# Performance work log

Measured on AMD Instinct MI355X. Metric: run time of the kernel, lower is better.

## Reference

```python
import jax, jax.numpy as jnp
import numpy as np

E = 32      # particle_embed_dim = q/k/v head out dim
G = 2       # nof_net_types (conv groups)
NEG_SLOPE = 0.01


def _glin(x, w, b, groups):
    """Grouped 1x1 conv on (M, C, 1, 1) == grouped linear.
    x: (M, Cin), w: (Cout, Cin//groups), b: (Cout,)."""
    M = x.shape[0]
    Cout = w.shape[0]
    xg = x.reshape(M, groups, -1)                 # (M, G, Cin/G)
    wg = w.reshape(groups, Cout // groups, -1)    # (G, Cout/G, Cin/G)
    y = jnp.einsum('mgi,goi->mgo', xg, wg).reshape(M, Cout)
    return y + b


def setup_inputs() -> dict:
    key = jax.random.key(0)
    ks = jax.random.split(key, 9)
    B, N = 32, 1024
    s = 0.05
    return {
        'x_e':   jax.random.normal(ks[0], (B, N, G * E), dtype=jnp.float32),
        'w_qkv': jax.random.normal(ks[1], (3 * G * E, E), dtype=jnp.float32) * s,
        'b_qkv': jax.random.normal(ks[2], (3 * G * E,), dtype=jnp.float32) * s,
        'w_h1':  jax.random.normal(ks[3], (G * E, 2 * E), dtype=jnp.float32) * s,
        'b_h1':  jax.random.normal(ks[4], (G * E,), dtype=jnp.float32) * s,
        'w_h10': jax.random.normal(ks[5], (G * E, E), dtype=jnp.float32) * s,
        'b_h10': jax.random.normal(ks[6], (G * E,), dtype=jnp.float32) * s,
        'w_h11': jax.random.normal(ks[7], (G * E, E), dtype=jnp.float32) * s,
        'b_h11': jax.random.normal(ks[8], (G * E,), dtype=jnp.float32) * s,
    }


def reference(x_e, w_qkv, b_qkv, w_h1, b_h1, w_h10, b_h10, w_h11, b_h11):
    B, N, D = x_e.shape                      # D = G*E = 64
    act = lambda z: jnp.where(z >= 0, z, NEG_SLOPE * z)

    # grouped 1x1-conv QKV projection
    qkv = _glin(x_e.reshape(B * N, D), w_qkv, b_qkv, G)        # (B*N, 3*G*E)
    qkv = qkv.reshape(B, N, G, 3, E).transpose(0, 2, 3, 1, 4)  # (B, G, 3, N, E)
    q, k, v = qkv[:, :, 0], qkv[:, :, 1], qkv[:, :, 2]         # each (B, G, N, E)

    # NOTE: module divides k by sqrt(E) and logits by sqrt(E) again -> 1/E total
    scale = 1.0 / E
    ip = jnp.einsum('bgne,bgme->bgnm', q, k) * scale           # (B, G, N, N)
    sip = jax.nn.softmax(ip, axis=-1)
    attn = jnp.einsum('bgnm,bgme->bgne', sip, v)               # (B, G, N, E)

    # concat pre-attention v with attention output, regroup per-particle
    x_xe = jnp.concatenate([v, attn], axis=3)                  # (B, G, N, 2E)
    x_xe = x_xe.transpose(0, 2, 1, 3).reshape(B * N, G * 2 * E)  # (B*N, 128)

    h = act(_glin(x_xe, w_h1, b_h1, G))
    h = act(_glin(h, w_h10, b_h10, G))
    h = act(_glin(h, w_h11, b_h11, G))
    return h.reshape(B * N, G * E, 1, 1)
```

## Files before the change

kernel.cpp:

```cpp
#include <hip/hip_runtime.h>

#define B_ 32
#define N_ 1024
#define NEG 0.01f
#define QSC (1.4426950408889634f/32.0f)

using half8  = __attribute__((ext_vector_type(8))) _Float16;
using half4  = __attribute__((ext_vector_type(4))) _Float16;
using floatx4 = __attribute__((ext_vector_type(4))) float;

#if defined(__has_builtin)
#if __has_builtin(__builtin_amdgcn_exp2f)
#define EXP2(x) __builtin_amdgcn_exp2f(x)
#endif
#endif
#ifndef EXP2
#define EXP2(x) exp2f(x)
#endif

__device__ inline half8 cvt8(float4 a, float4 b) {
    half8 h;
    h[0]=(_Float16)a.x; h[1]=(_Float16)a.y; h[2]=(_Float16)a.z; h[3]=(_Float16)a.w;
    h[4]=(_Float16)b.x; h[5]=(_Float16)b.y; h[6]=(_Float16)b.z; h[7]=(_Float16)b.w;
    return h;
}

struct __align__(16) Smem {
    _Float16 wsh[96*36];
    float    bsh[96];
    _Float16 Kst[128*40];
    _Float16 Vtst[32*136];
    union {
        _Float16 qs[128*40];
        _Float16 xs[128*72];
    } u;
    float linv[128];
    float bl1[32], bl10[32], bl11[32];
};

__global__ __launch_bounds__(256, 2) void fused_kernel(
    const float* __restrict__ x, const float* __restrict__ w_qkv, const float* __restrict__ b_qkv,
    const float* __restrict__ w_h1,  const float* __restrict__ b_h1,
    const float* __restrict__ w_h10, const float* __restrict__ b_h10,
    const float* __restrict__ w_h11, const float* __restrict__ b_h11,
    float* __restrict__ out)
{
    __shared__ Smem sm;
    int t = threadIdx.x;
    int bg = blockIdx.x >> 3;
    int qtile = blockIdx.x & 7;
    int b = bg >> 1, g = bg & 1;
    int qbase = qtile * 128;
    int lane = t & 63, w = t >> 6;
    int L15 = lane & 15, quad = lane >> 4;

    for (int idx = t; idx < 96*32; idx += 256) {
        int r = idx >> 5, c = idx & 31;
        sm.wsh[r*36 + c] = (_Float16)w_qkv[(g*96 + r)*32 + c];
    }
    if (t < 96) sm.bsh[t] = b_qkv[g*96 + t];
    if (t < 32) {
        sm.bl1[t]  = b_h1[g*32+t];
        sm.bl10[t] = b_h10[g*32+t];
        sm.bl11[t] = b_h11[g*32+t];
    }
    __syncthreads();

    half8 bwq[2], bwk[2], bwv[2];
    float bqv[2], bkv[2], bvv[2];
    #pragma unroll
    for (int et = 0; et < 2; et++) {
        bwq[et] = *(const half8*)&sm.wsh[(     et*16 + L15)*36 + quad*8];
        bwk[et] = *(const half8*)&sm.wsh[(32 + et*16 + L15)*36 + quad*8];
        bwv[et] = *(const half8*)&sm.wsh[(64 + et*16 + L15)*36 + quad*8];
        bqv[et] = sm.bsh[     et*16 + L15];
        bkv[et] = sm.bsh[32 + et*16 + L15];
        bvv[et] = sm.bsh[64 + et*16 + L15];
    }

    {
        floatx4 z = {0.f,0.f,0.f,0.f};
        floatx4 dq[2][2];
        #pragma unroll
        for (int mt = 0; mt < 2; mt++) {
            const float* p = x + ((size_t)b*N_ + qbase + w*32 + mt*16 + L15)*64 + g*32 + quad*8;
            float4 f0 = *(const float4*)p;
            float4 f1 = *(const float4*)(p + 4);
            half8 axq = cvt8(f0, f1);
            dq[mt][0] = __builtin_amdgcn_mfma_f32_16x16x32_f16(axq, bwq[0], z, 0,0,0);
            dq[mt][1] = __builtin_amdgcn_mfma_f32_16x16x32_f16(axq, bwq[1], z, 0,0,0);
        }
        #pragma unroll
        for (int mt = 0; mt < 2; mt++)
            #pragma unroll
            for (int et = 0; et < 2; et++)
                #pragma unroll
                for (int r = 0; r < 4; r++)
                    sm.u.qs[(w*32 + mt*16 + quad*4 + r)*40 + et*16 + L15] =
                        (_Float16)((dq[mt][et][r] + bqv[et])*QSC);
    }
    __syncthreads();
    half8 bq0 = *(const half8*)&sm.u.qs[(w*32 +      L15)*40 + quad*8];
    half8 bq1 = *(const half8*)&sm.u.qs[(w*32 + 16 + L15)*40 + quad*8];

    float4 xf0[2], xf1[2];
    #pragma unroll
    for (int mt = 0; mt < 2; mt++) {
        const float* p = x + ((size_t)b*N_ + 0*128 + w*32 + mt*16 + L15)*64 + g*32 + quad*8;
        xf0[mt] = *(const float4*)p;
        xf1[mt] = *(const float4*)(p + 4);
    }

    floatx4 o00 = {0.f,0.f,0.f,0.f}, o01 = o00, o10 = o00, o11 = o00;
    float lsum0 = 0.f, lsum1 = 0.f;

    for (int kt = 0; kt < 8; kt++) {
        floatx4 z = {0.f,0.f,0.f,0.f};
        floatx4 dK[2][2], dV[2][2];
        #pragma unroll
        for (int mt = 0; mt < 2; mt++) {
            half8 axk = cvt8(xf0[mt], xf1[mt]);
            dK[mt][0] = __builtin_amdgcn_mfma_f32_16x16x32_f16(axk, bwk[0], z, 0,0,0);
            dK[mt][1] = __builtin_amdgcn_mfma_f32_16x16x32_f16(axk, bwk[1], z, 0,0,0);
            dV[mt][0] = __builtin_amdgcn_mfma_f32_16x16x32_f16(axk, bwv[0], z, 0,0,0);
            dV[mt][1] = __builtin_amdgcn_mfma_f32_16x16x32_f16(axk, bwv[1], z, 0,0,0);
        }
        __syncthreads();
        #pragma unroll
        for (int mt = 0; mt < 2; mt++) {
            int rb = w*32 + mt*16 + quad*4;
            #pragma unroll
            for (int et = 0; et < 2; et++) {
                half4 vh;
                #pragma unroll
                for (int r = 0; r < 4; r++) {
                    sm.Kst[(rb + r)*40 + et*16 + L15] = (_Float16)(dK[mt][et][r] + bkv[et]);
                    vh[r] = (_Float16)(dV[mt][et][r] + bvv[et]);
                }
                *(half4*)&sm.Vtst[(et*16 + L15)*136 + rb] = vh;
                if (kt == qtile) {
                    #pragma unroll
                    for (int r = 0; r < 4; r++)
                        sm.u.xs[(rb + r)*72 + et*16 + L15] = vh[r];
                }
            }
        }
        __syncthreads();
        if (kt < 7) {
            #pragma unroll
            for (int mt = 0; mt < 2; mt++) {
                const float* p = x + ((size_t)b*N_ + (kt+1)*128 + w*32 + mt*16 + L15)*64 + g*32 + quad*8;
                xf0[mt] = *(const float4*)p;
                xf1[mt] = *(const float4*)(p + 4);
            }
        }
        #pragma unroll
        for (int mt8 = 0; mt8 < 8; mt8++) {
            half8 ak = *(const half8*)&sm.Kst[(mt8*16 + L15)*40 + quad*8];
            floatx4 zz = {0.f,0.f,0.f,0.f};
            floatx4 s0 = __builtin_amdgcn_mfma_f32_16x16x32_f16(ak, bq0, zz, 0,0,0);
            floatx4 s1 = __builtin_amdgcn_mfma_f32_16x16x32_f16(ak, bq1, zz, 0,0,0);
            float p00 = EXP2(s0.x), p01 = EXP2(s0.y), p02 = EXP2(s0.z), p03 = EXP2(s0.w);
            float p10 = EXP2(s1.x), p11 = EXP2(s1.y), p12 = EXP2(s1.z), p13 = EXP2(s1.w);
            lsum0 += (p00+p01)+(p02+p03);
            lsum1 += (p10+p11)+(p12+p13);
            half4 a0 = { (_Float16)p00, (_Float16)p01, (_Float16)p02, (_Float16)p03 };
            half4 a1 = { (_Float16)p10, (_Float16)p11, (_Float16)p12, (_Float16)p13 };
            half4 bv0 = *(const half4*)&sm.Vtst[      L15*136 + mt8*16 + quad*4];
            half4 bv1 = *(const half4*)&sm.Vtst[(16 + L15)*136 + mt8*16 + quad*4];
            o00 = __builtin_amdgcn_mfma_f32_16x16x16f16(a0, bv0, o00, 0,0,0);
            o01 = __builtin_amdgcn_mfma_f32_16x16x16f16(a0, bv1, o01, 0,0,0);
            o10 = __builtin_amdgcn_mfma_f32_16x16x16f16(a1, bv0, o10, 0,0,0);
            o11 = __builtin_amdgcn_mfma_f32_16x16x16f16(a1, bv1, o11, 0,0,0);
        }
    }

    lsum0 += __shfl_xor(lsum0, 16, 64); lsum0 += __shfl_xor(lsum0, 32, 64);
    lsum1 += __shfl_xor(lsum1, 16, 64); lsum1 += __shfl_xor(lsum1, 32, 64);
    if (quad == 0) {
        sm.linv[w*32 +      L15] = 1.0f / lsum0;
        sm.linv[w*32 + 16 + L15] = 1.0f / lsum1;
    }
    __syncthreads();

    {
        const floatx4* ofr[2][2] = { {&o00,&o01}, {&o10,&o11} };
        #pragma unroll
        for (int nt = 0; nt < 2; nt++) {
            float4 li = *(const float4*)&sm.linv[w*32 + nt*16 + quad*4];
            #pragma unroll
            for (int et = 0; et < 2; et++) {
                floatx4 ov = *ofr[nt][et];
                sm.u.xs[(w*32+nt*16+quad*4+0)*72 + 32 + et*16 + L15] = (_Float16)(ov[0]*li.x);
                sm.u.xs[(w*32+nt*16+quad*4+1)*72 + 32 + et*16 + L15] = (_Float16)(ov[1]*li.y);
                sm.u.xs[(w*32+nt*16+quad*4+2)*72 + 32 + et*16 + L15] = (_Float16)(ov[2]*li.z);
                sm.u.xs[(w*32+nt*16+quad*4+3)*72 + 32 + et*16 + L15] = (_Float16)(ov[3]*li.w);
            }
        }
    }
    __syncthreads();

    half4 a1f[2][4], a2f[2][2], a3f[2][2];
    #pragma unroll
    for (int mt = 0; mt < 2; mt++) {
        #pragma unroll
        for (int kt = 0; kt < 4; kt++) {
            float4 f = *(const float4*)(w_h1 + (size_t)(g*32+mt*16+L15)*64 + kt*16 + quad*4);
            half4 h = { (_Float16)f.x, (_Float16)f.y, (_Float16)f.z, (_Float16)f.w };
            a1f[mt][kt] = h;
        }
        #pragma unroll
        for (int kt = 0; kt < 2; kt++) {
            float4 f = *(const float4*)(w_h10 + (size_t)(g*32+mt*16+L15)*32 + kt*16 + quad*4);
            half4 h = { (_Float16)f.x, (_Float16)f.y, (_Float16)f.z, (_Float16)f.w };
            a2f[mt][kt] = h;
            float4 f2 = *(const float4*)(w_h11 + (size_t)(g*32+mt*16+L15)*32 + kt*16 + quad*4);
            half4 h2 = { (_Float16)f2.x, (_Float16)f2.y, (_Float16)f2.z, (_Float16)f2.w };
            a3f[mt][kt] = h2;
        }
    }

    floatx4 d1[2][2];
    #pragma unroll
    for (int mt = 0; mt < 2; mt++)
        #pragma unroll
        for (int nt = 0; nt < 2; nt++) d1[mt][nt] = (floatx4){0.f,0.f,0.f,0.f};
    #pragma unroll
    for (int nt = 0; nt < 2; nt++)
        #pragma unroll
        for (int kt = 0; kt < 4; kt++) {
            half4 b1 = *(const half4*)&sm.u.xs[(w*32+nt*16+L15)*72 + kt*16 + quad*4];
            d1[0][nt] = __builtin_amdgcn_mfma_f32_16x16x16f16(a1f[0][kt], b1, d1[0][nt], 0,0,0);
            d1[1][nt] = __builtin_amdgcn_mfma_f32_16x16x16f16(a1f[1][kt], b1, d1[1][nt], 0,0,0);
        }
    half4 h1b[2][2];
    #pragma unroll
    for (int mt = 0; mt < 2; mt++) {
        float4 bb = *(const float4*)&sm.bl1[mt*16 + quad*4];
        #pragma unroll
        for (int nt = 0; nt < 2; nt++) {
            float v0 = d1[mt][nt][0] + bb.x; v0 = (v0>=0.f)?v0:NEG*v0;
            float v1 = d1[mt][nt][1] + bb.y; v1 = (v1>=0.f)?v1:NEG*v1;
            float v2 = d1[mt][nt][2] + bb.z; v2 = (v2>=0.f)?v2:NEG*v2;
            float v3 = d1[mt][nt][3] + bb.w; v3 = (v3>=0.f)?v3:NEG*v3;
            half4 h = { (_Float16)v0, (_Float16)v1, (_Float16)v2, (_Float16)v3 };
            h1b[mt][nt] = h;
        }
    }
    floatx4 d2[2][2];
    #pragma unroll
    for (int mt = 0; mt < 2; mt++)
        #pragma unroll
        for (int nt = 0; nt < 2; nt++) d2[mt][nt] = (floatx4){0.f,0.f,0.f,0.f};
    #pragma unroll
    for (int mt = 0; mt < 2; mt++)
        #pragma unroll
        for (int nt = 0; nt < 2; nt++)
            #pragma unroll
            for (int kt = 0; kt < 2; kt++)
                d2[mt][nt] = __builtin_amdgcn_mfma_f32_16x16x16f16(a2f[mt][kt], h1b[kt][nt], d2[mt][nt], 0,0,0);
    half4 h2b[2][2];
    #pragma unroll
    for (int mt = 0; mt < 2; mt++) {
        float4 bb = *(const float4*)&sm.bl10[mt*16 + quad*4];
        #pragma unroll
        for (int nt = 0; nt < 2; nt++) {
            float v0 = d2[mt][nt][0] + bb.x; v0 = (v0>=0.f)?v0:NEG*v0;
            float v1 = d2[mt][nt][1] + bb.y; v1 = (v1>=0.f)?v1:NEG*v1;
            float v2 = d2[mt][nt][2] + bb.z; v2 = (v2>=0.f)?v2:NEG*v2;
            float v3 = d2[mt][nt][3] + bb.w; v3 = (v3>=0.f)?v3:NEG*v3;
            half4 h = { (_Float16)v0, (_Float16)v1, (_Float16)v2, (_Float16)v3 };
            h2b[mt][nt] = h;
        }
    }
    floatx4 d3[2][2];
    #pragma unroll
    for (int mt = 0; mt < 2; mt++)
        #pragma unroll
        for (int nt = 0; nt < 2; nt++) d3[mt][nt] = (floatx4){0.f,0.f,0.f,0.f};
    #pragma unroll
    for (int mt = 0; mt < 2; mt++)
        #pragma unroll
        for (int nt = 0; nt < 2; nt++)
            #pragma unroll
            for (int kt = 0; kt < 2; kt++)
                d3[mt][nt] = __builtin_amdgcn_mfma_f32_16x16x16f16(a3f[mt][kt], h2b[kt][nt], d3[mt][nt], 0,0,0);
    #pragma unroll
    for (int mt = 0; mt < 2; mt++) {
        float4 bb = *(const float4*)&sm.bl11[mt*16 + quad*4];
        #pragma unroll
        for (int nt = 0; nt < 2; nt++) {
            float4 ov;
            ov.x = d3[mt][nt][0] + bb.x; ov.x = (ov.x>=0.f)?ov.x:NEG*ov.x;
            ov.y = d3[mt][nt][1] + bb.y; ov.y = (ov.y>=0.f)?ov.y:NEG*ov.y;
            ov.z = d3[mt][nt][2] + bb.z; ov.z = (ov.z>=0.f)?ov.z:NEG*ov.z;
            ov.w = d3[mt][nt][3] + bb.w; ov.w = (ov.w>=0.f)?ov.w:NEG*ov.w;
            *(float4*)(out + ((size_t)b*N_ + qbase + w*32 + nt*16 + L15)*64 + g*32 + mt*16 + quad*4) = ov;
        }
    }
}

extern "C" void kernel_launch(void* const* d_in, const int* in_sizes, int n_in,
                              void* d_out, int out_size, void* d_ws, size_t ws_size,
                              hipStream_t stream) {
    const float* x_e   = (const float*)d_in[0];
    const float* w_qkv = (const float*)d_in[1];
    const float* b_qkv = (const float*)d_in[2];
    const float* w_h1  = (const float*)d_in[3];
    const float* b_h1  = (const float*)d_in[4];
    const float* w_h10 = (const float*)d_in[5];
    const float* b_h10 = (const float*)d_in[6];
    const float* w_h11 = (const float*)d_in[7];
    const float* b_h11 = (const float*)d_in[8];
    float* out = (float*)d_out;

    hipLaunchKernelGGL(fused_kernel, dim3(B_*2*8), dim3(256), 0, stream,
                       x_e, w_qkv, b_qkv, w_h1, b_h1, w_h10, b_h10, w_h11, b_h11, out);
}
```

Baseline: 100.1 us.

## Double-buffer K/V tiles in LDS, fold biases into MFMA accumulators, use packed fp16 converts

K/V shared-memory tiles are double-buffered so the projection of the next key tile runs after the current tile's attention MFMAs, leaving one barrier per iteration instead of two. Biases are now seeded into the MFMA accumulators, and the Q scale is folded into the Q weights and bias, which removes per-element adds and multiplies. Scalar float-to-half conversions are replaced with packed round-toward-zero conversions (cvt_pkrtz). The cost is extra LDS for the second buffers, which may affect the 2-blocks-per-CU occupancy, plus a small rounding-mode difference.

```diff
diff --git a/kernel.cpp b/kernel.cpp
--- a/kernel.cpp
+++ b/kernel.cpp
@@ -7,6 +7,8 @@
 
 using half8  = __attribute__((ext_vector_type(8))) _Float16;
 using half4  = __attribute__((ext_vector_type(4))) _Float16;
+using half2  = __attribute__((ext_vector_type(2))) _Float16;
+using fp16x2 = __attribute__((ext_vector_type(2))) __fp16;
 using floatx4 = __attribute__((ext_vector_type(4))) float;
 
 #if defined(__has_builtin)
@@ -18,18 +20,25 @@
 #define EXP2(x) exp2f(x)
 #endif
 
+__device__ inline half2 pkcvt(float a, float b) {
+    fp16x2 r = __builtin_amdgcn_cvt_pkrtz(a, b);
+    return __builtin_bit_cast(half2, r);
+}
+
 __device__ inline half8 cvt8(float4 a, float4 b) {
-    half8 h;
-    h[0]=(_Float16)a.x; h[1]=(_Float16)a.y; h[2]=(_Float16)a.z; h[3]=(_Float16)a.w;
-    h[4]=(_Float16)b.x; h[5]=(_Float16)b.y; h[6]=(_Float16)b.z; h[7]=(_Float16)b.w;
+    half2 p0 = pkcvt(a.x, a.y);
+    half2 p1 = pkcvt(a.z, a.w);
+    half2 p2 = pkcvt(b.x, b.y);
+    half2 p3 = pkcvt(b.z, b.w);
+    half8 h = { p0[0],p0[1], p1[0],p1[1], p2[0],p2[1], p3[0],p3[1] };
     return h;
 }
 
 struct __align__(16) Smem {
     _Float16 wsh[96*36];
     float    bsh[96];
-    _Float16 Kst[128*40];
-    _Float16 Vtst[32*136];
+    _Float16 Kst[2][128*40];
+    _Float16 Vtst[2][32*136];
     union {
         _Float16 qs[128*40];
         _Float16 xs[128*72];
@@ -56,7 +65,8 @@
 
     for (int idx = t; idx < 96*32; idx += 256) {
         int r = idx >> 5, c = idx & 31;
-        sm.wsh[r*36 + c] = (_Float16)w_qkv[(g*96 + r)*32 + c];
+        float wv = w_qkv[(g*96 + r)*32 + c];
+        sm.wsh[r*36 + c] = (_Float16)(r < 32 ? wv*QSC : wv);
     }
     if (t < 96) sm.bsh[t] = b_qkv[g*96 + t];
     if (t < 32) {
@@ -67,28 +77,28 @@
     __syncthreads();
 
     half8 bwq[2], bwk[2], bwv[2];
-    float bqv[2], bkv[2], bvv[2];
+    floatx4 cq[2], ck[2], cv[2];
     #pragma unroll
     for (int et = 0; et < 2; et++) {
         bwq[et] = *(const half8*)&sm.wsh[(     et*16 + L15)*36 + quad*8];
         bwk[et] = *(const half8*)&sm.wsh[(32 + et*16 + L15)*36 + quad*8];
         bwv[et] = *(const half8*)&sm.wsh[(64 + et*16 + L15)*36 + quad*8];
-        bqv[et] = sm.bsh[     et*16 + L15];
-        bkv[et] = sm.bsh[32 + et*16 + L15];
-        bvv[et] = sm.bsh[64 + et*16 + L15];
+        float bq = sm.bsh[     et*16 + L15] * QSC;
+        float bk = sm.bsh[32 + et*16 + L15];
+        float bv = sm.bsh[64 + et*16 + L15];
+        cq[et] = (floatx4){bq,bq,bq,bq};
+        ck[et] = (floatx4){bk,bk,bk,bk};
+        cv[et] = (floatx4){bv,bv,bv,bv};
     }
 
     {
-        floatx4 z = {0.f,0.f,0.f,0.f};
         floatx4 dq[2][2];
         #pragma unroll
         for (int mt = 0; mt < 2; mt++) {
             const float* p = x + ((size_t)b*N_ + qbase + w*32 + mt*16 + L15)*64 + g*32 + quad*8;
-            float4 f0 = *(const float4*)p;
-            float4 f1 = *(const float4*)(p + 4);
-            half8 axq = cvt8(f0, f1);
-            dq[mt][0] = __builtin_amdgcn_mfma_f32_16x16x32_f16(axq, bwq[0], z, 0,0,0);
-            dq[mt][1] = __builtin_amdgcn_mfma_f32_16x16x32_f16(axq, bwq[1], z, 0,0,0);
+            half8 axq = cvt8(*(const float4*)p, *(const float4*)(p + 4));
+            dq[mt][0] = __builtin_amdgcn_mfma_f32_16x16x32_f16(axq, bwq[0], cq[0], 0,0,0);
+            dq[mt][1] = __builtin_amdgcn_mfma_f32_16x16x32_f16(axq, bwq[1], cq[1], 0,0,0);
         }
         #pragma unroll
         for (int mt = 0; mt < 2; mt++)
@@ -97,66 +107,68 @@
                 #pragma unroll
                 for (int r = 0; r < 4; r++)
                     sm.u.qs[(w*32 + mt*16 + quad*4 + r)*40 + et*16 + L15] =
-                        (_Float16)((dq[mt][et][r] + bqv[et])*QSC);
+                        (_Float16)dq[mt][et][r];
     }
     __syncthreads();
     half8 bq0 = *(const half8*)&sm.u.qs[(w*32 +      L15)*40 + quad*8];
     half8 bq1 = *(const half8*)&sm.u.qs[(w*32 + 16 + L15)*40 + quad*8];
 
     float4 xf0[2], xf1[2];
-    #pragma unroll
-    for (int mt = 0; mt < 2; mt++) {
-        const float* p = x + ((size_t)b*N_ + 0*128 + w*32 + mt*16 + L15)*64 + g*32 + quad*8;
-        xf0[mt] = *(const float4*)p;
-        xf1[mt] = *(const float4*)(p + 4);
-    }
-
-    floatx4 o00 = {0.f,0.f,0.f,0.f}, o01 = o00, o10 = o00, o11 = o00;
-    float lsum0 = 0.f, lsum1 = 0.f;
-
-    for (int kt = 0; kt < 8; kt++) {
-        floatx4 z = {0.f,0.f,0.f,0.f};
+    auto prefetch = [&](int tile) {
+        #pragma unroll
+        for (int mt = 0; mt < 2; mt++) {
+            const float* p = x + ((size_t)b*N_ + tile*128 + w*32 + mt*16 + L15)*64 + g*32 + quad*8;
+            xf0[mt] = *(const float4*)p;
+            xf1[mt] = *(const float4*)(p + 4);
+        }
+    };
+    auto proj_tile = [&](int tile, int buf) {
         floatx4 dK[2][2], dV[2][2];
         #pragma unroll
         for (int mt = 0; mt < 2; mt++) {
             half8 axk = cvt8(xf0[mt], xf1[mt]);
-            dK[mt][0] = __builtin_amdgcn_mfma_f32_16x16x32_f16(axk, bwk[0], z, 0,0,0);
-            dK[mt][1] = __builtin_amdgcn_mfma_f32_16x16x32_f16(axk, bwk[1], z, 0,0,0);
-            dV[mt][0] = __builtin_amdgcn_mfma_f32_16x16x32_f16(axk, bwv[0], z, 0,0,0);
-            dV[mt][1] = __builtin_amdgcn_mfma_f32_16x16x32_f16(axk, bwv[1], z, 0,0,0);
-        }
-        __syncthreads();
+            dK[mt][0] = __builtin_amdgcn_mfma_f32_16x16x32_f16(axk, bwk[0], ck[0], 0,0,0);
+            dK[mt][1] = __builtin_amdgcn_mfma_f32_16x16x32_f16(axk, bwk[1], ck[1], 0,0,0);
+            dV[mt][0] = __builtin_amdgcn_mfma_f32_16x16x32_f16(axk, bwv[0], cv[0], 0,0,0);
+            dV[mt][1] = __builtin_amdgcn_mfma_f32_16x16x32_f16(axk, bwv[1], cv[1], 0,0,0);
+        }
         #pragma unroll
         for (int mt = 0; mt < 2; mt++) {
             int rb = w*32 + mt*16 + quad*4;
             #pragma unroll
             for (int et = 0; et < 2; et++) {
-                half4 vh;
-                #pragma unroll
-                for (int r = 0; r < 4; r++) {
-                    sm.Kst[(rb + r)*40 + et*16 + L15] = (_Float16)(dK[mt][et][r] + bkv[et]);
-                    vh[r] = (_Float16)(dV[mt][et][r] + bvv[et]);
-                }
-                *(half4*)&sm.Vtst[(et*16 + L15)*136 + rb] = vh;
-                if (kt == qtile) {
+                half2 k01 = pkcvt(dK[mt][et][0], dK[mt][et][1]);
+                half2 k23 = pkcvt(dK[mt][et][2], dK[mt][et][3]);
+                half2 v01 = pkcvt(dV[mt][et][0], dV[mt][et][1]);
+                half2 v23 = pkcvt(dV[mt][et][2], dV[mt][et][3]);
+                half4 vh = { v01[0], v01[1], v23[0], v23[1] };
+                sm.Kst[buf][(rb+0)*40 + et*16 + L15] = k01[0];
+                sm.Kst[buf][(rb+1)*40 + et*16 + L15] = k01[1];
+                sm.Kst[buf][(rb+2)*40 + et*16 + L15] = k23[0];
+                sm.Kst[buf][(rb+3)*40 + et*16 + L15] = k23[1];
+                *(half4*)&sm.Vtst[buf][(et*16 + L15)*136 + rb] = vh;
+                if (tile == qtile) {
                     #pragma unroll
                     for (int r = 0; r < 4; r++)
                         sm.u.xs[(rb + r)*72 + et*16 + L15] = vh[r];
                 }
             }
         }
-        __syncthreads();
-        if (kt < 7) {
-            #pragma unroll
-            for (int mt = 0; mt < 2; mt++) {
-                const float* p = x + ((size_t)b*N_ + (kt+1)*128 + w*32 + mt*16 + L15)*64 + g*32 + quad*8;
-                xf0[mt] = *(const float4*)p;
-                xf1[mt] = *(const float4*)(p + 4);
-            }
-        }
+    };
+
+    prefetch(0);
+    proj_tile(0, 0);
+    __syncthreads();
+
+    floatx4 o00 = {0.f,0.f,0.f,0.f}, o01 = o00, o10 = o00, o11 = o00;
+    float lsum0 = 0.f, lsum1 = 0.f;
+
+    for (int kt = 0; kt < 8; kt++) {
+        int cur = kt & 1;
+        if (kt < 7) prefetch(kt + 1);
         #pragma unroll
         for (int mt8 = 0; mt8 < 8; mt8++) {
-            half8 ak = *(const half8*)&sm.Kst[(mt8*16 + L15)*40 + quad*8];
+            half8 ak = *(const half8*)&sm.Kst[cur][(mt8*16 + L15)*40 + quad*8];
             floatx4 zz = {0.f,0.f,0.f,0.f};
             floatx4 s0 = __builtin_amdgcn_mfma_f32_16x16x32_f16(ak, bq0, zz, 0,0,0);
             floatx4 s1 = __builtin_amdgcn_mfma_f32_16x16x32_f16(ak, bq1, zz, 0,0,0);
@@ -164,15 +176,21 @@
             float p10 = EXP2(s1.x), p11 = EXP2(s1.y), p12 = EXP2(s1.z), p13 = EXP2(s1.w);
             lsum0 += (p00+p01)+(p02+p03);
             lsum1 += (p10+p11)+(p12+p13);
-            half4 a0 = { (_Float16)p00, (_Float16)p01, (_Float16)p02, (_Float16)p03 };
-            half4 a1 = { (_Float16)p10, (_Float16)p11, (_Float16)p12, (_Float16)p13 };
-            half4 bv0 = *(const half4*)&sm.Vtst[      L15*136 + mt8*16 + quad*4];
-            half4 bv1 = *(const half4*)&sm.Vtst[(16 + L15)*136 + mt8*16 + quad*4];
+            half2 pa = pkcvt(p00, p01);
+            half2 pb = pkcvt(p02, p03);
+            half2 pc = pkcvt(p10, p11);
+            half2 pd = pkcvt(p12, p13);
+            half4 a0 = { pa[0], pa[1], pb[0], pb[1] };
+            half4 a1 = { pc[0], pc[1], pd[0], pd[1] };
+            half4 bv0 = *(const half4*)&sm.Vtst[cur][      L15*136 + mt8*16 + quad*4];
+            half4 bv1 = *(const half4*)&sm.Vtst[cur][(16 + L15)*136 + mt8*16 + quad*4];
             o00 = __builtin_amdgcn_mfma_f32_16x16x16f16(a0, bv0, o00, 0,0,0);
             o01 = __builtin_amdgcn_mfma_f32_16x16x16f16(a0, bv1, o01, 0,0,0);
             o10 = __builtin_amdgcn_mfma_f32_16x16x16f16(a1, bv0, o10, 0,0,0);
             o11 = __builtin_amdgcn_mfma_f32_16x16x16f16(a1, bv1, o11, 0,0,0);
         }
+        if (kt < 7) proj_tile(kt + 1, 1 - cur);
+        __syncthreads();
     }
 
     lsum0 += __shfl_xor(lsum0, 16, 64); lsum0 += __shfl_xor(lsum0, 32, 64);
@@ -206,25 +224,33 @@
         #pragma unroll
         for (int kt = 0; kt < 4; kt++) {
             float4 f = *(const float4*)(w_h1 + (size_t)(g*32+mt*16+L15)*64 + kt*16 + quad*4);
-            half4 h = { (_Float16)f.x, (_Float16)f.y, (_Float16)f.z, (_Float16)f.w };
+            half2 ha = pkcvt(f.x, f.y);
+            half2 hb = pkcvt(f.z, f.w);
+            half4 h = { ha[0], ha[1], hb[0], hb[1] };
             a1f[mt][kt] = h;
         }
         #pragma unroll
         for (int kt = 0; kt < 2; kt++) {
             float4 f = *(const float4*)(w_h10 + (size_t)(g*32+mt*16+L15)*32 + kt*16 + quad*4);
-            half4 h = { (_Float16)f.x, (_Float16)f.y, (_Float16)f.z, (_Float16)f.w };
+            half2 ha = pkcvt(f.x, f.y);
+            half2 hb = pkcvt(f.z, f.w);
+            half4 h = { ha[0], ha[1], hb[0], hb[1] };
             a2f[mt][kt] = h;
             float4 f2 = *(const float4*)(w_h11 + (size_t)(g*32+mt*16+L15)*32 + kt*16 + quad*4);
-            half4 h2 = { (_Float16)f2.x, (_Float16)f2.y, (_Float16)f2.z, (_Float16)f2.w };
+            half2 hc = pkcvt(f2.x, f2.y);
+            half2 hd = pkcvt(f2.z, f2.w);
+            half4 h2 = { hc[0], hc[1], hd[0], hd[1] };
             a3f[mt][kt] = h2;
         }
     }
 
     floatx4 d1[2][2];
     #pragma unroll
-    for (int mt = 0; mt < 2; mt++)
-        #pragma unroll
-        for (int nt = 0; nt < 2; nt++) d1[mt][nt] = (floatx4){0.f,0.f,0.f,0.f};
+    for (int mt = 0; mt < 2; mt++) {
+        float4 bb = *(const float4*)&sm.bl1[mt*16 + quad*4];
+        floatx4 seed = { bb.x, bb.y, bb.z, bb.w };
+        d1[mt][0] = seed; d1[mt][1] = seed;
+    }
     #pragma unroll
     for (int nt = 0; nt < 2; nt++)
         #pragma unroll
@@ -235,23 +261,25 @@
         }
     half4 h1b[2][2];
     #pragma unroll
+    for (int mt = 0; mt < 2; mt++)
+        #pragma unroll
+        for (int nt = 0; nt < 2; nt++) {
+            float v0 = d1[mt][nt][0]; v0 = (v0>=0.f)?v0:NEG*v0;
+            float v1 = d1[mt][nt][1]; v1 = (v1>=0.f)?v1:NEG*v1;
+            float v2 = d1[mt][nt][2]; v2 = (v2>=0.f)?v2:NEG*v2;
+            float v3 = d1[mt][nt][3]; v3 = (v3>=0.f)?v3:NEG*v3;
+            half2 ha = pkcvt(v0, v1);
+            half2 hb = pkcvt(v2, v3);
+            half4 h = { ha[0], ha[1], hb[0], hb[1] };
+            h1b[mt][nt] = h;
+        }
+    floatx4 d2[2][2];
+    #pragma unroll
     for (int mt = 0; mt < 2; mt++) {
-        float4 bb = *(const float4*)&sm.bl1[mt*16 + quad*4];
-        #pragma unroll
-        for (int nt = 0; nt < 2; nt++) {
-            float v0 = d1[mt][nt][0] + bb.x; v0 = (v0>=0.f)?v0:NEG*v0;
-            float v1 = d1[mt][nt][1] + bb.y; v1 = (v1>=0.f)?v1:NEG*v1;
-            float v2 = d1[mt][nt][2] + bb.z; v2 = (v2>=0.f)?v2:NEG*v2;
-            float v3 = d1[mt][nt][3] + bb.w; v3 = (v3>=0.f)?v3:NEG*v3;
-            half4 h = { (_Float16)v0, (_Float16)v1, (_Float16)v2, (_Float16)v3 };
-            h1b[mt][nt] = h;
-        }
-    }
-    floatx4 d2[2][2];
-    #pragma unroll
-    for (int mt = 0; mt < 2; mt++)
-        #pragma unroll
-        for (int nt = 0; nt < 2; nt++) d2[mt][nt] = (floatx4){0.f,0.f,0.f,0.f};
+        float4 bb = *(const float4*)&sm.bl10[mt*16 + quad*4];
+        floatx4 seed = { bb.x, bb.y, bb.z, bb.w };
+        d2[mt][0] = seed; d2[mt][1] = seed;
+    }
     #pragma unroll
     for (int mt = 0; mt < 2; mt++)
         #pragma unroll
@@ -261,23 +289,25 @@
                 d2[mt][nt] = __builtin_amdgcn_mfma_f32_16x16x16f16(a2f[mt][kt], h1b[kt][nt], d2[mt][nt], 0,0,0);
     half4 h2b[2][2];
     #pragma unroll
+    for (int mt = 0; mt < 2; mt++)
+        #pragma unroll
+        for (int nt = 0; nt < 2; nt++) {
+            float v0 = d2[mt][nt][0]; v0 = (v0>=0.f)?v0:NEG*v0;
+            float v1 = d2[mt][nt][1]; v1 = (v1>=0.f)?v1:NEG*v1;
+            float v2 = d2[mt][nt][2]; v2 = (v2>=0.f)?v2:NEG*v2;
+            float v3 = d2[mt][nt][3]; v3 = (v3>=0.f)?v3:NEG*v3;
+            half2 ha = pkcvt(v0, v1);
+            half2 hb = pkcvt(v2, v3);
+            half4 h = { ha[0], ha[1], hb[0], hb[1] };
+            h2b[mt][nt] = h;
+        }
+    floatx4 d3[2][2];
+    #pragma unroll
     for (int mt = 0; mt < 2; mt++) {
-        float4 bb = *(const float4*)&sm.bl10[mt*16 + quad*4];
-        #pragma unroll
-        for (int nt = 0; nt < 2; nt++) {
-            float v0 = d2[mt][nt][0] + bb.x; v0 = (v0>=0.f)?v0:NEG*v0;
-            float v1 = d2[mt][nt][1] + bb.y; v1 = (v1>=0.f)?v1:NEG*v1;
-            float v2 = d2[mt][nt][2] + bb.z; v2 = (v2>=0.f)?v2:NEG*v2;
-            float v3 = d2[mt][nt][3] + bb.w; v3 = (v3>=0.f)?v3:NEG*v3;
-            half4 h = { (_Float16)v0, (_Float16)v1, (_Float16)v2, (_Float16)v3 };
-            h2b[mt][nt] = h;
-        }
-    }
-    floatx4 d3[2][2];
-    #pragma unroll
-    for (int mt = 0; mt < 2; mt++)
-        #pragma unroll
-        for (int nt = 0; nt < 2; nt++) d3[mt][nt] = (floatx4){0.f,0.f,0.f,0.f};
+        float4 bb = *(const float4*)&sm.bl11[mt*16 + quad*4];
+        floatx4 seed = { bb.x, bb.y, bb.z, bb.w };
+        d3[mt][0] = seed; d3[mt][1] = seed;
+    }
     #pragma unroll
     for (int mt = 0; mt < 2; mt++)
         #pragma unroll
@@ -286,18 +316,16 @@
             for (int kt = 0; kt < 2; kt++)
                 d3[mt][nt] = __builtin_amdgcn_mfma_f32_16x16x16f16(a3f[mt][kt], h2b[kt][nt], d3[mt][nt], 0,0,0);
     #pragma unroll
-    for (int mt = 0; mt < 2; mt++) {
-        float4 bb = *(const float4*)&sm.bl11[mt*16 + quad*4];
+    for (int mt = 0; mt < 2; mt++)
         #pragma unroll
         for (int nt = 0; nt < 2; nt++) {
             float4 ov;
-            ov.x = d3[mt][nt][0] + bb.x; ov.x = (ov.x>=0.f)?ov.x:NEG*ov.x;
-            ov.y = d3[mt][nt][1] + bb.y; ov.y = (ov.y>=0.f)?ov.y:NEG*ov.y;
-            ov.z = d3[mt][nt][2] + bb.z; ov.z = (ov.z>=0.f)?ov.z:NEG*ov.z;
-            ov.w = d3[mt][nt][3] + bb.w; ov.w = (ov.w>=0.f)?ov.w:NEG*ov.w;
+            ov.x = d3[mt][nt][0]; ov.x = (ov.x>=0.f)?ov.x:NEG*ov.x;
+            ov.y = d3[mt][nt][1]; ov.y = (ov.y>=0.f)?ov.y:NEG*ov.y;
+            ov.z = d3[mt][nt][2]; ov.z = (ov.z>=0.f)?ov.z:NEG*ov.z;
+            ov.w = d3[mt][nt][3]; ov.w = (ov.w>=0.f)?ov.w:NEG*ov.w;
             *(float4*)(out + ((size_t)b*N_ + qbase + w*32 + nt*16 + L15)*64 + g*32 + mt*16 + quad*4) = ov;
         }
-    }
 }
 
 extern "C" void kernel_launch(void* const* d_in, const int* in_sizes, int n_in,
```

After: 98.57 us. Within noise of the previous version (-1.6%).
